# Optimization experiments

Measured on AMD Instinct MI355X. Metric: run time of the kernel, lower is better.

## Reference

```python
import jax, jax.numpy as jnp
import numpy as np

NS, NV = 48, 10            # scalar / vector multiplicities
IN_SIZE = NS + 3*NV + 3*NV + NS   # 156
N_EDGE_FEAT = 96
HIDDEN = 96
# weight shapes per output irrep: 0e:(58,48) 1o:(68,10) 1e:(68,10) 0o:(58,48)
W_SHAPES = [('0e', NS + NV, NS), ('1o', NS + 2*NV, NV), ('1e', 2*NV + NS, NV), ('0o', NV + NS, NS)]
WEIGHT_NUMEL = sum(a*b for _, a, b in W_SHAPES)  # 6928
N_NODES, N_EDGES = 10000, 50000


def setup_inputs() -> dict:
    key = jax.random.key(0)
    ks = jax.random.split(key, 9)
    node_attr = jax.random.normal(ks[0], (N_NODES, IN_SIZE), dtype=jnp.float32)
    edge_index = jax.random.randint(ks[1], (2, N_EDGES), 0, N_NODES)
    edge_attr = jax.random.normal(ks[2], (N_EDGES, N_EDGE_FEAT), dtype=jnp.float32)
    edge_sh = jax.random.normal(ks[3], (N_EDGES, 4), dtype=jnp.float32)
    s1 = 1.0 / np.sqrt(N_EDGE_FEAT)
    s2 = 1.0 / np.sqrt(HIDDEN)
    W1 = jax.random.normal(ks[4], (N_EDGE_FEAT, HIDDEN), dtype=jnp.float32) * s1
    b1 = jnp.zeros((HIDDEN,), dtype=jnp.float32)
    W2 = jax.random.normal(ks[5], (HIDDEN, WEIGHT_NUMEL), dtype=jnp.float32) * s2
    b2 = jnp.zeros((WEIGHT_NUMEL,), dtype=jnp.float32)
    return {'node_attr': node_attr, 'edge_index': edge_index, 'edge_attr': edge_attr,
            'edge_sh': edge_sh, 'W1': W1, 'b1': b1, 'W2': W2, 'b2': b2}


def _faster_tp(in_, sh, weight):
    # in_: [E, 156], sh: [E, 4], weight: [E, 6928]
    in_0e = in_[:, :NS]                                   # [E,48]
    in_1o = in_[:, NS:NS + 3*NV].reshape(-1, NV, 3)       # [E,10,3]
    in_1e = in_[:, NS + 3*NV:NS + 6*NV].reshape(-1, NV, 3)
    in_0o = in_[:, NS + 6*NV:]                            # [E,48]
    sh_0e = sh[:, 0]                                      # [E]
    sh_1o = sh[:, 1:]                                     # [E,3]
    inv_s3 = 1.0 / np.sqrt(3.0)
    inv_s2 = 1.0 / np.sqrt(2.0)

    out_0e = jnp.concatenate([
        in_0e * sh_0e[:, None],
        jnp.sum(in_1o * sh_1o[:, None, :], axis=-1) * inv_s3], axis=-1)      # [E,58]
    out_1o = jnp.concatenate([
        in_0e[:, :, None] * sh_1o[:, None, :],
        in_1o * sh_0e[:, None, None],
        jnp.cross(in_1e, sh_1o[:, None, :]) * inv_s2], axis=-2)              # [E,68,3]
    out_1e = jnp.concatenate([
        jnp.cross(in_1o, sh_1o[:, None, :]) * inv_s2,
        in_1e * sh_0e[:, None, None],
        in_0o[:, :, None] * sh_1o[:, None, :]], axis=-2)                     # [E,68,3]
    out_0o = jnp.concatenate([
        jnp.sum(in_1e * sh_1o[:, None, :], axis=-1) * inv_s3,
        in_0o * sh_0e[:, None]], axis=-1)                                    # [E,58]

    wd = {}
    start = 0
    for name, a, b in W_SHAPES:
        wd[name] = weight[:, start:start + a*b].reshape(-1, a, b) / np.sqrt(a)
        start += a*b

    o0e = jnp.einsum('ei,eio->eo', out_0e, wd['0e'])                 # [E,48]
    o1o = jnp.einsum('eic,eio->eoc', out_1o, wd['1o']).reshape(-1, 3*NV)
    o1e = jnp.einsum('eic,eio->eoc', out_1e, wd['1e']).reshape(-1, 3*NV)
    o0o = jnp.einsum('ei,eio->eo', out_0o, wd['0o'])                 # [E,48]
    return jnp.concatenate([o0e, o1o, o1e, o0o], axis=-1)           # [E,156]


def reference(node_attr, edge_index, edge_attr, edge_sh, W1, b1, W2, b2):
    edge_src, edge_dst = edge_index[0], edge_index[1]
    # edge MLP -> per-edge TP weights
    h = jax.nn.relu(edge_attr @ W1 + b1)
    w = h @ W2 + b2                                       # [E, 6928]
    tp = _faster_tp(node_attr[edge_dst], edge_sh, w)      # [E, 156]
    # scatter-mean over source nodes
    n = node_attr.shape[0]
    seg = jax.ops.segment_sum(tp, edge_src, num_segments=n)
    cnt = jax.ops.segment_sum(jnp.ones((tp.shape[0],), tp.dtype), edge_src, num_segments=n)
    out = seg / jnp.maximum(cnt, 1.0)[:, None]
    # residual (in/out sizes equal, so pad is a no-op)
    return out + node_attr
```

## Files before the change

### kernel.cpp

```cpp
#include <hip/hip_runtime.h>

#define NE 50000
#define NN 10000
#define KH 96
#define WN 6928
#define NTILE 484
#define IN_SZ 156
#define EPW 32

typedef __attribute__((ext_vector_type(8))) short short8;
typedef __attribute__((ext_vector_type(4))) float float4v;

__device__ __forceinline__ unsigned short f2bf(float x) {
  unsigned u = __float_as_uint(x);
  unsigned r = (u + 0x7FFFu + ((u >> 16) & 1u)) >> 16;
  return (unsigned short)r;
}
__device__ __forceinline__ float b2f(unsigned short u) {
  return __uint_as_float(((unsigned)u) << 16);
}

__device__ __forceinline__ void issue3(short8 (&B)[3], float &bv,
                                       const unsigned short* p, const float* pb) {
  asm volatile("global_load_dwordx4 %0, %4, off\n\t"
               "global_load_dwordx4 %1, %4, off offset:1024\n\t"
               "global_load_dwordx4 %2, %4, off offset:2048\n\t"
               "global_load_dword %3, %5, off"
               : "=&v"(B[0]), "=&v"(B[1]), "=&v"(B[2]), "=&v"(bv)
               : "v"(p), "v"(pb));
}
__device__ __forceinline__ void waitB8(short8 (&B)[3], float &bv) {
  asm volatile("s_waitcnt vmcnt(8)"
               : "+v"(B[0]), "+v"(B[1]), "+v"(B[2]), "+v"(bv));
}
__device__ __forceinline__ void waitB4(short8 (&B)[3], float &bv) {
  asm volatile("s_waitcnt vmcnt(4)"
               : "+v"(B[0]), "+v"(B[1]), "+v"(B[2]), "+v"(bv));
}
__device__ __forceinline__ void waitB0(short8 (&B)[3], float &bv) {
  asm volatile("s_waitcnt vmcnt(0)"
               : "+v"(B[0]), "+v"(B[1]), "+v"(B[2]), "+v"(bv));
}

__device__ __forceinline__ int col_of_np(int np) {
  if (np < 2784) return np;
  if (np < 3872) { int rel = np - 2784, i = rel >> 4, o = rel & 15; return (o < 10) ? 2784 + i * 10 + o : -1; }
  if (np < 4960) { int rel = np - 3872, i = rel >> 4, o = rel & 15; return (o < 10) ? 3464 + i * 10 + o : -1; }
  return 4144 + (np - 4960);
}

__global__ __launch_bounds__(256) void w1t_kernel(
    const float* __restrict__ W1, unsigned short* __restrict__ W1T)
{
  int j = blockIdx.x * 256 + threadIdx.x;
  if (j < KH * KH) {
    int c = j / KH, k = j - c * KH;
    W1T[c * KH + k] = f2bf(W1[k * KH + c]);
  }
}

__global__ __launch_bounds__(384) void mlp1_kernel(
    const float* __restrict__ edge_attr, const unsigned short* __restrict__ W1T,
    const float* __restrict__ b1, unsigned short* __restrict__ h_ext)
{
  const int tid = threadIdx.x;
  const int e0 = blockIdx.x * 16;
  const int w = tid >> 6, l = tid & 15, q = (tid >> 4) & 3;

  short8 a[3], b[3];
  #pragma unroll
  for (int s = 0; s < 3; ++s) {
    const float* pa = edge_attr + (size_t)(e0 + l) * KH + s * 32 + q * 8;
    float4 x = *(const float4*)pa, y = *(const float4*)(pa + 4);
    short8 t;
    t[0] = (short)f2bf(x.x); t[1] = (short)f2bf(x.y);
    t[2] = (short)f2bf(x.z); t[3] = (short)f2bf(x.w);
    t[4] = (short)f2bf(y.x); t[5] = (short)f2bf(y.y);
    t[6] = (short)f2bf(y.z); t[7] = (short)f2bf(y.w);
    a[s] = t;
    b[s] = *(const short8*)(W1T + (size_t)(w * 16 + l) * KH + s * 32 + q * 8);
  }
  float4v C = {0.f, 0.f, 0.f, 0.f};
  #pragma unroll
  for (int s = 0; s < 3; ++s)
    C = __builtin_amdgcn_mfma_f32_16x16x32_bf16(a[s], b[s], C, 0, 0, 0);

  float bv = b1[w * 16 + l];
  #pragma unroll
  for (int r = 0; r < 4; ++r)
    h_ext[(size_t)(e0 + q * 4 + r) * KH + w * 16 + l] = f2bf(fmaxf(C[r] + bv, 0.f));
}

__global__ __launch_bounds__(256) void w2pt_kernel(
    const float* __restrict__ W2, const float* __restrict__ b2,
    unsigned short* __restrict__ W2PT, float* __restrict__ b2PT)
{
  int gid = blockIdx.x * 256 + threadIdx.x;
  if (gid < NTILE * 192) {
    int lane = gid & 63, s = (gid >> 6) % 3, t = gid / 192;
    int l = lane & 15, q = lane >> 4;
    int c = col_of_np(t * 16 + l);
    int kbase = s * 32 + q * 8;
    unsigned short o8[8];
    #pragma unroll
    for (int j = 0; j < 8; ++j) {
      int k = kbase + j;
      float v = (c >= 0) ? W2[(size_t)k * WN + c] : 0.f;
      o8[j] = f2bf(v);
    }
    uint4 pk;
    pk.x = o8[0] | ((unsigned)o8[1] << 16);
    pk.y = o8[2] | ((unsigned)o8[3] << 16);
    pk.z = o8[4] | ((unsigned)o8[5] << 16);
    pk.w = o8[6] | ((unsigned)o8[7] << 16);
    *(uint4*)(W2PT + (size_t)gid * 8) = pk;
  } else {
    int j = gid - NTILE * 192;
    if (j < NTILE * 16) {
      int c = col_of_np(j);
      b2PT[j] = (c >= 0) ? b2[c] : 0.f;
    }
  }
}

__global__ __launch_bounds__(512, 4) void tp_kernel(
    const unsigned short* __restrict__ h_ext, const float* __restrict__ node_attr,
    const int* __restrict__ edge_index, const float* __restrict__ edge_sh,
    const unsigned short* __restrict__ W2PT, const float* __restrict__ b2PT,
    float* __restrict__ acc, int* __restrict__ icnt)
{
  __shared__ unsigned short sIn[EPW][160];
  __shared__ float sOut[EPW][IN_SZ];
  __shared__ unsigned short sF0[2][60][EPW];
  __shared__ unsigned short sF1[2][68][3][EPW];
  __shared__ float sShs[EPW][4];
  __shared__ int sSrc[EPW], sDst[EPW];

  const int tid = threadIdx.x;
  const int e0 = blockIdx.x * EPW;

  if (tid < EPW) {
    int ok = (e0 + tid) < NE;
    int s = ok ? edge_index[e0 + tid] : 0;
    int d = ok ? edge_index[NE + e0 + tid] : 0;
    sSrc[tid] = s; sDst[tid] = d;
    if (ok) atomicAdd(&icnt[s], 1);
  }
  if (tid >= 128 && tid < 256) {
    int t2 = tid - 128;
    int e = t2 >> 2, c = t2 & 3;
    sShs[e][c] = ((e0 + e) < NE) ? edge_sh[(size_t)(e0 + e) * 4 + c] : 0.f;
  }
  __syncthreads();

  for (int idx = tid; idx < EPW * IN_SZ; idx += 512) {
    int e = idx / IN_SZ, f = idx - e * IN_SZ;
    sIn[e][f] = f2bf(node_attr[(size_t)sDst[e] * IN_SZ + f]);
  }
  for (int idx = tid; idx < EPW * IN_SZ; idx += 512) (&sOut[0][0])[idx] = 0.f;
  __syncthreads();

  {
    const int e = tid >> 4, j = tid & 15;
    const float sh0 = sShs[e][0], sx = sShs[e][1], sy = sShs[e][2], sz = sShs[e][3];
    const float i3 = 0.57735026918962576f, i2 = 0.70710678118654752f;
    for (int i = j; i < 48; i += 16) {
      float v0 = b2f(sIn[e][i]), w0 = b2f(sIn[e][108 + i]);
      sF0[0][i][e] = f2bf(v0 * sh0);
      sF0[1][10 + i][e] = f2bf(w0 * sh0);
      sF1[0][i][0][e] = f2bf(v0 * sx); sF1[0][i][1][e] = f2bf(v0 * sy); sF1[0][i][2][e] = f2bf(v0 * sz);
      sF1[1][20 + i][0][e] = f2bf(w0 * sx); sF1[1][20 + i][1][e] = f2bf(w0 * sy); sF1[1][20 + i][2][e] = f2bf(w0 * sz);
    }
    if (j < 10) {
      const int v = j;
      float ax = b2f(sIn[e][48 + 3 * v]), ay = b2f(sIn[e][48 + 3 * v + 1]), az = b2f(sIn[e][48 + 3 * v + 2]);
      float bx = b2f(sIn[e][78 + 3 * v]), by = b2f(sIn[e][78 + 3 * v + 1]), bz = b2f(sIn[e][78 + 3 * v + 2]);
      sF0[0][48 + v][e] = f2bf((ax * sx + ay * sy + az * sz) * i3);
      sF0[1][v][e]      = f2bf((bx * sx + by * sy + bz * sz) * i3);
      sF1[0][48 + v][0][e] = f2bf(ax * sh0); sF1[0][48 + v][1][e] = f2bf(ay * sh0); sF1[0][48 + v][2][e] = f2bf(az * sh0);
      sF1[0][58 + v][0][e] = f2bf((by * sz - bz * sy) * i2);
      sF1[0][58 + v][1][e] = f2bf((bz * sx - bx * sz) * i2);
      sF1[0][58 + v][2][e] = f2bf((bx * sy - by * sx) * i2);
      sF1[1][v][0][e] = f2bf((ay * sz - az * sy) * i2);
      sF1[1][v][1][e] = f2bf((az * sx - ax * sz) * i2);
      sF1[1][v][2][e] = f2bf((ax * sy - ay * sx) * i2);
      sF1[1][10 + v][0][e] = f2bf(bx * sh0); sF1[1][10 + v][1][e] = f2bf(by * sh0); sF1[1][10 + v][2][e] = f2bf(bz * sh0);
    }
  }
  if (tid < 128) {
    int fam = tid >> 6, i = 58 + ((tid >> 5) & 1), e = tid & 31;
    sF0[fam][i][e] = 0;
  }
  __syncthreads();

  const int wv = tid >> 6, l = tid & 15, q = (tid >> 4) & 3;

  short8 Af[2][3];
  #pragma unroll
  for (int m = 0; m < 2; ++m) {
    const unsigned short* ar = h_ext + (size_t)(e0 + m * 16 + l) * KH + q * 8;
    #pragma unroll
    for (int s = 0; s < 3; ++s) Af[m][s] = *(const short8*)(ar + s * 32);
  }

  const unsigned short* wlane = W2PT + (size_t)(tid & 63) * 8;
  const float* blane = b2PT + l;

  if (wv < 4) {
    const int sf = wv >> 1;
    const int ibeg = (wv & 1) * 30;
    const int tb = sf ? 310 : 0;
    const int obase = sf ? 108 : 0;
    #pragma unroll 1
    for (int ob = 0; ob < 3; ++ob) {
      float a0[4] = {0.f, 0.f, 0.f, 0.f}, a1[4] = {0.f, 0.f, 0.f, 0.f};
      short8 Ba[3], Bb[3], Bc[3];
      float vA, vB, vC;
      auto taddr = [&](int ii) -> size_t {
        int i = ibeg + ii; if (i >= 58) i = ibeg;
        return (size_t)(tb + 3 * i + ob);
      };
      auto body = [&](const short8 (&B)[3], float bv, int ii) {
        int i = ibeg + ii;
        ushort4 f0 = *(const ushort4*)&sF0[sf][i][q * 4];
        ushort4 f1 = *(const ushort4*)&sF0[sf][i][16 + q * 4];
        float4v C0 = {bv, bv, bv, bv}, C1 = {bv, bv, bv, bv};
        #pragma unroll
        for (int s = 0; s < 3; ++s) {
          C0 = __builtin_amdgcn_mfma_f32_16x16x32_bf16(Af[0][s], B[s], C0, 0, 0, 0);
          C1 = __builtin_amdgcn_mfma_f32_16x16x32_bf16(Af[1][s], B[s], C1, 0, 0, 0);
        }
        a0[0] += C0[0] * b2f(f0.x); a0[1] += C0[1] * b2f(f0.y);
        a0[2] += C0[2] * b2f(f0.z); a0[3] += C0[3] * b2f(f0.w);
        a1[0] += C1[0] * b2f(f1.x); a1[1] += C1[1] * b2f(f1.y);
        a1[2] += C1[2] * b2f(f1.z); a1[3] += C1[3] * b2f(f1.w);
      };
      { size_t t = taddr(0); issue3(Ba, vA, wlane + t * 1536, blane + t * 16); }
      { size_t t = taddr(1); issue3(Bb, vB, wlane + t * 1536, blane + t * 16); }
      { size_t t = taddr(2); issue3(Bc, vC, wlane + t * 1536, blane + t * 16); }
      #pragma unroll 1
      for (int ii = 0; ii < 27; ii += 3) {
        waitB8(Ba, vA); body(Ba, vA, ii);
        { size_t t = taddr(ii + 3); issue3(Ba, vA, wlane + t * 1536, blane + t * 16); }
        waitB8(Bb, vB); body(Bb, vB, ii + 1);
        { size_t t = taddr(ii + 4); issue3(Bb, vB, wlane + t * 1536, blane + t * 16); }
        waitB8(Bc, vC); body(Bc, vC, ii + 2);
        { size_t t = taddr(ii + 5); issue3(Bc, vC, wlane + t * 1536, blane + t * 16); }
      }
      waitB8(Ba, vA); body(Ba, vA, 27);
      waitB4(Bb, vB); body(Bb, vB, 28);
      waitB0(Bc, vC); body(Bc, vC, 29);
      const int col = obase + ob * 16 + l;
      #pragma unroll
      for (int r = 0; r < 4; ++r) {
        unsafeAtomicAdd(&sOut[q * 4 + r][col], a0[r]);
        unsafeAtomicAdd(&sOut[16 + q * 4 + r][col], a1[r]);
      }
    }
  } else {
    const int vf = (wv >> 1) - 2;
    const int ibeg = (wv & 1) * 34;
    const int tb = vf ? 242 : 174;
    float r0[4][3] = {{0.f}}, r1[4][3] = {{0.f}};
    short8 Ba[3], Bb[3];
    float vA, vB;
    auto tadr = [&](int ii) -> size_t { return (size_t)(tb + ibeg + ii); };
    auto body = [&](const short8 (&B)[3], float bv, int ii) {
      int i = ibeg + ii;
      ushort4 g0[3], g1[3];
      #pragma unroll
      for (int cc = 0; cc < 3; ++cc) {
        g0[cc] = *(const ushort4*)&sF1[vf][i][cc][q * 4];
        g1[cc] = *(const ushort4*)&sF1[vf][i][cc][16 + q * 4];
      }
      float4v C0 = {bv, bv, bv, bv}, C1 = {bv, bv, bv, bv};
      #pragma unroll
      for (int s = 0; s < 3; ++s) {
        C0 = __builtin_amdgcn_mfma_f32_16x16x32_bf16(Af[0][s], B[s], C0, 0, 0, 0);
        C1 = __builtin_amdgcn_mfma_f32_16x16x32_bf16(Af[1][s], B[s], C1, 0, 0, 0);
      }
      #pragma unroll
      for (int cc = 0; cc < 3; ++cc) {
        r0[0][cc] += C0[0] * b2f(g0[cc].x); r0[1][cc] += C0[1] * b2f(g0[cc].y);
        r0[2][cc] += C0[2] * b2f(g0[cc].z); r0[3][cc] += C0[3] * b2f(g0[cc].w);
        r1[0][cc] += C1[0] * b2f(g1[cc].x); r1[1][cc] += C1[1] * b2f(g1[cc].y);
        r1[2][cc] += C1[2] * b2f(g1[cc].z); r1[3][cc] += C1[3] * b2f(g1[cc].w);
      }
    };
    { size_t t = tadr(0); issue3(Ba, vA, wlane + t * 1536, blane + t * 16); }
    { size_t t = tadr(1); issue3(Bb, vB, wlane + t * 1536, blane + t * 16); }
    #pragma unroll 1
    for (int ii = 0; ii < 32; ii += 2) {
      waitB4(Ba, vA); body(Ba, vA, ii);
      { size_t t = tadr(ii + 2); issue3(Ba, vA, wlane + t * 1536, blane + t * 16); }
      waitB4(Bb, vB); body(Bb, vB, ii + 1);
      { size_t t = tadr(ii + 3); issue3(Bb, vB, wlane + t * 1536, blane + t * 16); }
    }
    waitB4(Ba, vA); body(Ba, vA, 32);
    waitB0(Bb, vB); body(Bb, vB, 33);
    if (l < 10) {
      const int col = (vf ? 78 : 48) + 3 * l;
      #pragma unroll
      for (int r = 0; r < 4; ++r)
        #pragma unroll
        for (int cc = 0; cc < 3; ++cc) {
          unsafeAtomicAdd(&sOut[q * 4 + r][col + cc], r0[r][cc]);
          unsafeAtomicAdd(&sOut[16 + q * 4 + r][col + cc], r1[r][cc]);
        }
    }
  }
  __syncthreads();

  const float n58 = 0.13130643285972254f, n68 = 0.12126781251816650f;
  for (int idx = tid; idx < EPW * IN_SZ; idx += 512) {
    int e = idx / IN_SZ, o = idx - e * IN_SZ;
    if (e0 + e < NE) {
      float nrm = (o < 48 || o >= 108) ? n58 : n68;
      unsafeAtomicAdd(&acc[(size_t)sSrc[e] * IN_SZ + o], sOut[e][o] * nrm);
    }
  }
}

__global__ __launch_bounds__(256) void finalize_kernel(
    const float* __restrict__ acc, const int* __restrict__ icnt,
    const float* __restrict__ node_attr, float* __restrict__ out)
{
  int idx = blockIdx.x * 256 + threadIdx.x;
  if (idx < NN * IN_SZ) {
    int n = idx / IN_SZ;
    out[idx] = acc[idx] / fmaxf((float)icnt[n], 1.f) + node_attr[idx];
  }
}

extern "C" void kernel_launch(void* const* d_in, const int* in_sizes, int n_in,
                              void* d_out, int out_size, void* d_ws, size_t ws_size,
                              hipStream_t stream)
{
  const float* node_attr  = (const float*)d_in[0];
  const int*   edge_index = (const int*)d_in[1];
  const float* edge_attr  = (const float*)d_in[2];
  const float* edge_sh    = (const float*)d_in[3];
  const float* W1 = (const float*)d_in[4];
  const float* b1 = (const float*)d_in[5];
  const float* W2 = (const float*)d_in[6];
  const float* b2 = (const float*)d_in[7];
  float* out = (float*)d_out;

  unsigned short* h_ext = (unsigned short*)d_ws;
  unsigned short* W2PT  = h_ext + (size_t)50016 * KH;
  float* b2PT = (float*)(W2PT + (size_t)NTILE * 1536);
  float* acc  = b2PT + (size_t)NTILE * 16;
  int*   icnt = (int*)(acc + (size_t)NN * IN_SZ);
  unsigned short* W1T = (unsigned short*)(icnt + NN);

  w1t_kernel<<<(KH * KH + 255) / 256, 256, 0, stream>>>(W1, W1T);
  w2pt_kernel<<<(NTILE * 208 + 255) / 256, 256, 0, stream>>>(W2, b2, W2PT, b2PT);
  mlp1_kernel<<<NE / 16, 384, 0, stream>>>(edge_attr, W1T, b1, h_ext);
  hipMemsetAsync(acc, 0, (size_t)NN * IN_SZ * sizeof(float), stream);
  hipMemsetAsync(icnt, 0, (size_t)NN * sizeof(int), stream);
  hipMemsetAsync(h_ext + (size_t)NE * KH, 0, (size_t)16 * KH * sizeof(unsigned short), stream);
  tp_kernel<<<(NE + EPW - 1) / EPW, 512, 0, stream>>>(h_ext, node_attr, edge_index,
                                                      edge_sh, W2PT, b2PT, acc, icnt);
  finalize_kernel<<<(NN * IN_SZ + 255) / 256, 256, 0, stream>>>(acc, icnt, node_attr, out);
}
```

Before: 312.3 us.

## Quantize hidden activations and W2 to int8 and use i8 MFMA in TP kernel

Hidden activations are now quantized per edge and W2 per column to int8 with scales, and the per-edge weight GEMM uses int8 MFMA with int32 accumulation, followed by dequantization and bias. This halves weight and activation bytes and uses the higher-throughput int8 matrix path. The weight-transpose, W2 packing and memsets are also merged into a single prep kernel to cut launches. Occupancy hint changes from 4 to 2 waves per SIMD, and int8 quantization adds accuracy risk relative to bf16.

```diff
diff --git a/kernel.cpp b/kernel.cpp
--- a/kernel.cpp
+++ b/kernel.cpp
@@ -10,6 +10,9 @@
 
 typedef __attribute__((ext_vector_type(8))) short short8;
 typedef __attribute__((ext_vector_type(4))) float float4v;
+typedef __attribute__((ext_vector_type(4))) int int4v;
+typedef __attribute__((ext_vector_type(2))) float float2v;
+typedef __attribute__((ext_vector_type(2))) long long2v;
 
 __device__ __forceinline__ unsigned short f2bf(float x) {
   unsigned u = __float_as_uint(x);
@@ -19,27 +22,31 @@
 __device__ __forceinline__ float b2f(unsigned short u) {
   return __uint_as_float(((unsigned)u) << 16);
 }
-
-__device__ __forceinline__ void issue3(short8 (&B)[3], float &bv,
-                                       const unsigned short* p, const float* pb) {
-  asm volatile("global_load_dwordx4 %0, %4, off\n\t"
-               "global_load_dwordx4 %1, %4, off offset:1024\n\t"
-               "global_load_dwordx4 %2, %4, off offset:2048\n\t"
-               "global_load_dword %3, %5, off"
-               : "=&v"(B[0]), "=&v"(B[1]), "=&v"(B[2]), "=&v"(bv)
-               : "v"(p), "v"(pb));
-}
-__device__ __forceinline__ void waitB8(short8 (&B)[3], float &bv) {
-  asm volatile("s_waitcnt vmcnt(8)"
-               : "+v"(B[0]), "+v"(B[1]), "+v"(B[2]), "+v"(bv));
-}
-__device__ __forceinline__ void waitB4(short8 (&B)[3], float &bv) {
-  asm volatile("s_waitcnt vmcnt(4)"
-               : "+v"(B[0]), "+v"(B[1]), "+v"(B[2]), "+v"(bv));
-}
-__device__ __forceinline__ void waitB0(short8 (&B)[3], float &bv) {
-  asm volatile("s_waitcnt vmcnt(0)"
-               : "+v"(B[0]), "+v"(B[1]), "+v"(B[2]), "+v"(bv));
+__device__ __forceinline__ unsigned char q8(float x, float inv) {
+  return (unsigned char)(signed char)__float2int_rn(fminf(fmaxf(x * inv, -127.f), 127.f));
+}
+__device__ __forceinline__ unsigned p4(unsigned a, unsigned b, unsigned c, unsigned d) {
+  return a | (b << 8) | (c << 16) | (d << 24);
+}
+
+__device__ __forceinline__ void issueT(long2v &W01, long &W2f, float2v &bs,
+                                       const unsigned char* pA,
+                                       const unsigned char* pB,
+                                       const float* pbs) {
+  asm volatile("global_load_dwordx4 %0, %3, off\n\t"
+               "global_load_dwordx2 %1, %4, off\n\t"
+               "global_load_dwordx2 %2, %5, off"
+               : "=&v"(W01), "=&v"(W2f), "=&v"(bs)
+               : "v"(pA), "v"(pB), "v"(pbs));
+}
+__device__ __forceinline__ void waitT6(long2v &W01, long &W2f, float2v &bs) {
+  asm volatile("s_waitcnt vmcnt(6)" : "+v"(W01), "+v"(W2f), "+v"(bs));
+}
+__device__ __forceinline__ void waitT3(long2v &W01, long &W2f, float2v &bs) {
+  asm volatile("s_waitcnt vmcnt(3)" : "+v"(W01), "+v"(W2f), "+v"(bs));
+}
+__device__ __forceinline__ void waitT0(long2v &W01, long &W2f, float2v &bs) {
+  asm volatile("s_waitcnt vmcnt(0)" : "+v"(W01), "+v"(W2f), "+v"(bs));
 }
 
 __device__ __forceinline__ int col_of_np(int np) {
@@ -49,23 +56,83 @@
   return 4144 + (np - 4960);
 }
 
-__global__ __launch_bounds__(256) void w1t_kernel(
-    const float* __restrict__ W1, unsigned short* __restrict__ W1T)
+#define R0 (NTILE * 16)
+#define R1 (R0 + KH * KH)
+#define R2 (R1 + NN * IN_SZ / 4)
+#define R3 (R2 + NN / 4)
+#define R4 (R3 + 96)
+#define R5 (R4 + 4)
+__global__ __launch_bounds__(256) void prep_kernel(
+    const float* __restrict__ W2, const float* __restrict__ b2,
+    const float* __restrict__ W1,
+    unsigned char* __restrict__ W2PT8, float2v* __restrict__ bscPT,
+    unsigned short* __restrict__ W1T,
+    float* __restrict__ acc, int* __restrict__ icnt,
+    unsigned char* __restrict__ h8, float* __restrict__ hscale)
 {
-  int j = blockIdx.x * 256 + threadIdx.x;
-  if (j < KH * KH) {
+  int gid = blockIdx.x * 256 + threadIdx.x;
+  if (gid < R0) {
+    int np = gid, t = np >> 4, l = np & 15;
+    int c = col_of_np(np);
+    float m = 0.f;
+    if (c >= 0) {
+      #pragma unroll 1
+      for (int k = 0; k < KH; ++k) m = fmaxf(m, fabsf(W2[(size_t)k * WN + c]));
+    }
+    float sc = m / 127.f;
+    float inv = (m > 0.f) ? 127.f / m : 0.f;
+    float2v bs; bs.x = (c >= 0) ? b2[c] : 0.f; bs.y = sc;
+    bscPT[np] = bs;
+    #pragma unroll 1
+    for (int qq = 0; qq < 4; ++qq) {
+      unsigned char bb[24];
+      #pragma unroll
+      for (int j = 0; j < 8; ++j) {
+        int k0 = qq * 8 + j;
+        bb[j]      = q8((c >= 0) ? W2[(size_t)k0 * WN + c] : 0.f, inv);
+        bb[8 + j]  = q8((c >= 0) ? W2[(size_t)(32 + k0) * WN + c] : 0.f, inv);
+        bb[16 + j] = q8((c >= 0) ? W2[(size_t)(64 + k0) * WN + c] : 0.f, inv);
+      }
+      uint4 pa;
+      pa.x = p4(bb[0], bb[1], bb[2], bb[3]);
+      pa.y = p4(bb[4], bb[5], bb[6], bb[7]);
+      pa.z = p4(bb[8], bb[9], bb[10], bb[11]);
+      pa.w = p4(bb[12], bb[13], bb[14], bb[15]);
+      *(uint4*)(W2PT8 + (size_t)t * 1536 + (qq * 16 + l) * 16) = pa;
+      uint2 pb;
+      pb.x = p4(bb[16], bb[17], bb[18], bb[19]);
+      pb.y = p4(bb[20], bb[21], bb[22], bb[23]);
+      *(uint2*)(W2PT8 + (size_t)t * 1536 + 1024 + (qq * 16 + l) * 8) = pb;
+    }
+  } else if (gid < R1) {
+    int j = gid - R0;
     int c = j / KH, k = j - c * KH;
     W1T[c * KH + k] = f2bf(W1[k * KH + c]);
+  } else if (gid < R2) {
+    uint4 z = {0, 0, 0, 0};
+    ((uint4*)acc)[gid - R1] = z;
+  } else if (gid < R3) {
+    uint4 z = {0, 0, 0, 0};
+    ((uint4*)icnt)[gid - R2] = z;
+  } else if (gid < R4) {
+    uint4 z = {0, 0, 0, 0};
+    ((uint4*)(h8 + (size_t)NE * KH))[gid - R3] = z;
+  } else if (gid < R5) {
+    uint4 z = {0, 0, 0, 0};
+    ((uint4*)(hscale + NE))[gid - R4] = z;
   }
 }
 
 __global__ __launch_bounds__(384) void mlp1_kernel(
     const float* __restrict__ edge_attr, const unsigned short* __restrict__ W1T,
-    const float* __restrict__ b1, unsigned short* __restrict__ h_ext)
+    const float* __restrict__ b1, unsigned char* __restrict__ h8,
+    float* __restrict__ hscale)
 {
+  __shared__ unsigned rmax[16];
   const int tid = threadIdx.x;
   const int e0 = blockIdx.x * 16;
   const int w = tid >> 6, l = tid & 15, q = (tid >> 4) & 3;
+  if (tid < 16) rmax[tid] = 0;
 
   short8 a[3], b[3];
   #pragma unroll
@@ -86,47 +153,32 @@
     C = __builtin_amdgcn_mfma_f32_16x16x32_bf16(a[s], b[s], C, 0, 0, 0);
 
   float bv = b1[w * 16 + l];
-  #pragma unroll
-  for (int r = 0; r < 4; ++r)
-    h_ext[(size_t)(e0 + q * 4 + r) * KH + w * 16 + l] = f2bf(fmaxf(C[r] + bv, 0.f));
-}
-
-__global__ __launch_bounds__(256) void w2pt_kernel(
-    const float* __restrict__ W2, const float* __restrict__ b2,
-    unsigned short* __restrict__ W2PT, float* __restrict__ b2PT)
-{
-  int gid = blockIdx.x * 256 + threadIdx.x;
-  if (gid < NTILE * 192) {
-    int lane = gid & 63, s = (gid >> 6) % 3, t = gid / 192;
-    int l = lane & 15, q = lane >> 4;
-    int c = col_of_np(t * 16 + l);
-    int kbase = s * 32 + q * 8;
-    unsigned short o8[8];
+  float v[4];
+  #pragma unroll
+  for (int r = 0; r < 4; ++r) v[r] = fmaxf(C[r] + bv, 0.f);
+  __syncthreads();
+  #pragma unroll
+  for (int r = 0; r < 4; ++r) atomicMax(&rmax[q * 4 + r], __float_as_uint(v[r]));
+  __syncthreads();
+  #pragma unroll
+  for (int r = 0; r < 4; ++r) {
+    float m = __uint_as_float(rmax[q * 4 + r]);
+    float inv = (m > 0.f) ? 127.f / m : 0.f;
+    h8[(size_t)(e0 + q * 4 + r) * KH + w * 16 + l] =
+        (unsigned char)__float2int_rn(v[r] * inv);
+  }
+  if (w == 0 && l == 0) {
     #pragma unroll
-    for (int j = 0; j < 8; ++j) {
-      int k = kbase + j;
-      float v = (c >= 0) ? W2[(size_t)k * WN + c] : 0.f;
-      o8[j] = f2bf(v);
-    }
-    uint4 pk;
-    pk.x = o8[0] | ((unsigned)o8[1] << 16);
-    pk.y = o8[2] | ((unsigned)o8[3] << 16);
-    pk.z = o8[4] | ((unsigned)o8[5] << 16);
-    pk.w = o8[6] | ((unsigned)o8[7] << 16);
-    *(uint4*)(W2PT + (size_t)gid * 8) = pk;
-  } else {
-    int j = gid - NTILE * 192;
-    if (j < NTILE * 16) {
-      int c = col_of_np(j);
-      b2PT[j] = (c >= 0) ? b2[c] : 0.f;
-    }
-  }
-}
-
-__global__ __launch_bounds__(512, 4) void tp_kernel(
-    const unsigned short* __restrict__ h_ext, const float* __restrict__ node_attr,
+    for (int r = 0; r < 4; ++r)
+      hscale[e0 + q * 4 + r] = __uint_as_float(rmax[q * 4 + r]) / 127.f;
+  }
+}
+
+__global__ __launch_bounds__(512, 2) void tp_kernel(
+    const unsigned char* __restrict__ h8, const float* __restrict__ node_attr,
     const int* __restrict__ edge_index, const float* __restrict__ edge_sh,
-    const unsigned short* __restrict__ W2PT, const float* __restrict__ b2PT,
+    const unsigned char* __restrict__ W2PT8, const float2v* __restrict__ bscPT,
+    const float* __restrict__ hscale,
     float* __restrict__ acc, int* __restrict__ icnt)
 {
   __shared__ unsigned short sIn[EPW][160];
@@ -195,16 +247,47 @@
 
   const int wv = tid >> 6, l = tid & 15, q = (tid >> 4) & 3;
 
-  short8 Af[2][3];
+  long Af[2][3];
+  float se0[4], se1[4];
   #pragma unroll
   for (int m = 0; m < 2; ++m) {
-    const unsigned short* ar = h_ext + (size_t)(e0 + m * 16 + l) * KH + q * 8;
+    const unsigned char* ar = h8 + (size_t)(e0 + m * 16 + l) * KH + q * 8;
     #pragma unroll
-    for (int s = 0; s < 3; ++s) Af[m][s] = *(const short8*)(ar + s * 32);
-  }
-
-  const unsigned short* wlane = W2PT + (size_t)(tid & 63) * 8;
-  const float* blane = b2PT + l;
+    for (int s = 0; s < 3; ++s) Af[m][s] = *(const long*)(ar + s * 32);
+  }
+  #pragma unroll
+  for (int r = 0; r < 4; ++r) {
+    se0[r] = hscale[e0 + q * 4 + r];
+    se1[r] = hscale[e0 + 16 + q * 4 + r];
+  }
+
+  const unsigned char* wlaneA = W2PT8 + (size_t)(tid & 63) * 16;
+  const unsigned char* wlaneB = W2PT8 + 1024 + (size_t)(tid & 63) * 8;
+  const float* bslane = (const float*)(bscPT + l);
+
+  auto sbody = [&](float (&a0)[4], float (&a1)[4],
+                   const long2v &W01, const long &W2f, const float2v &bs,
+                   int sf, int i) {
+    ushort4 f0 = *(const ushort4*)&sF0[sf][i][q * 4];
+    ushort4 f1 = *(const ushort4*)&sF0[sf][i][16 + q * 4];
+    int4v C0 = {0, 0, 0, 0}, C1 = {0, 0, 0, 0};
+    C0 = __builtin_amdgcn_mfma_i32_16x16x32_i8(Af[0][0], W01.x, C0, 0, 0, 0);
+    C1 = __builtin_amdgcn_mfma_i32_16x16x32_i8(Af[1][0], W01.x, C1, 0, 0, 0);
+    C0 = __builtin_amdgcn_mfma_i32_16x16x32_i8(Af[0][1], W01.y, C0, 0, 0, 0);
+    C1 = __builtin_amdgcn_mfma_i32_16x16x32_i8(Af[1][1], W01.y, C1, 0, 0, 0);
+    C0 = __builtin_amdgcn_mfma_i32_16x16x32_i8(Af[0][2], W2f, C0, 0, 0, 0);
+    C1 = __builtin_amdgcn_mfma_i32_16x16x32_i8(Af[1][2], W2f, C1, 0, 0, 0);
+    const float bv = bs.x, sc = bs.y;
+    float u;
+    u = fmaf((float)C0[0], sc * se0[0], bv); a0[0] = fmaf(u, b2f(f0.x), a0[0]);
+    u = fmaf((float)C0[1], sc * se0[1], bv); a0[1] = fmaf(u, b2f(f0.y), a0[1]);
+    u = fmaf((float)C0[2], sc * se0[2], bv); a0[2] = fmaf(u, b2f(f0.z), a0[2]);
+    u = fmaf((float)C0[3], sc * se0[3], bv); a0[3] = fmaf(u, b2f(f0.w), a0[3]);
+    u = fmaf((float)C1[0], sc * se1[0], bv); a1[0] = fmaf(u, b2f(f1.x), a1[0]);
+    u = fmaf((float)C1[1], sc * se1[1], bv); a1[1] = fmaf(u, b2f(f1.y), a1[1]);
+    u = fmaf((float)C1[2], sc * se1[2], bv); a1[2] = fmaf(u, b2f(f1.z), a1[2]);
+    u = fmaf((float)C1[3], sc * se1[3], bv); a1[3] = fmaf(u, b2f(f1.w), a1[3]);
+  };
 
   if (wv < 4) {
     const int sf = wv >> 1;
@@ -214,46 +297,30 @@
     #pragma unroll 1
     for (int ob = 0; ob < 3; ++ob) {
       float a0[4] = {0.f, 0.f, 0.f, 0.f}, a1[4] = {0.f, 0.f, 0.f, 0.f};
-      short8 Ba[3], Bb[3], Bc[3];
-      float vA, vB, vC;
-      auto taddr = [&](int ii) -> size_t {
+      long2v Wa01, Wb01, Wc01; long Wa2, Wb2, Wc2; float2v vA, vB, vC;
+      auto tadr = [&](int ii) -> size_t {
         int i = ibeg + ii; if (i >= 58) i = ibeg;
         return (size_t)(tb + 3 * i + ob);
       };
-      auto body = [&](const short8 (&B)[3], float bv, int ii) {
-        int i = ibeg + ii;
-        ushort4 f0 = *(const ushort4*)&sF0[sf][i][q * 4];
-        ushort4 f1 = *(const ushort4*)&sF0[sf][i][16 + q * 4];
-        float4v C0 = {bv, bv, bv, bv}, C1 = {bv, bv, bv, bv};
-        #pragma unroll
-        for (int s = 0; s < 3; ++s) {
-          C0 = __builtin_amdgcn_mfma_f32_16x16x32_bf16(Af[0][s], B[s], C0, 0, 0, 0);
-          C1 = __builtin_amdgcn_mfma_f32_16x16x32_bf16(Af[1][s], B[s], C1, 0, 0, 0);
-        }
-        a0[0] += C0[0] * b2f(f0.x); a0[1] += C0[1] * b2f(f0.y);
-        a0[2] += C0[2] * b2f(f0.z); a0[3] += C0[3] * b2f(f0.w);
-        a1[0] += C1[0] * b2f(f1.x); a1[1] += C1[1] * b2f(f1.y);
-        a1[2] += C1[2] * b2f(f1.z); a1[3] += C1[3] * b2f(f1.w);
-      };
-      { size_t t = taddr(0); issue3(Ba, vA, wlane + t * 1536, blane + t * 16); }
-      { size_t t = taddr(1); issue3(Bb, vB, wlane + t * 1536, blane + t * 16); }
-      { size_t t = taddr(2); issue3(Bc, vC, wlane + t * 1536, blane + t * 16); }
+      { size_t t = tadr(0); issueT(Wa01, Wa2, vA, wlaneA + t * 1536, wlaneB + t * 1536, bslane + t * 32); }
+      { size_t t = tadr(1); issueT(Wb01, Wb2, vB, wlaneA + t * 1536, wlaneB + t * 1536, bslane + t * 32); }
+      { size_t t = tadr(2); issueT(Wc01, Wc2, vC, wlaneA + t * 1536, wlaneB + t * 1536, bslane + t * 32); }
       #pragma unroll 1
       for (int ii = 0; ii < 27; ii += 3) {
-        waitB8(Ba, vA); body(Ba, vA, ii);
-        { size_t t = taddr(ii + 3); issue3(Ba, vA, wlane + t * 1536, blane + t * 16); }
-        waitB8(Bb, vB); body(Bb, vB, ii + 1);
-        { size_t t = taddr(ii + 4); issue3(Bb, vB, wlane + t * 1536, blane + t * 16); }
-        waitB8(Bc, vC); body(Bc, vC, ii + 2);
-        { size_t t = taddr(ii + 5); issue3(Bc, vC, wlane + t * 1536, blane + t * 16); }
-      }
-      waitB8(Ba, vA); body(Ba, vA, 27);
-      waitB4(Bb, vB); body(Bb, vB, 28);
-      waitB0(Bc, vC); body(Bc, vC, 29);
+        waitT6(Wa01, Wa2, vA); sbody(a0, a1, Wa01, Wa2, vA, sf, ibeg + ii);
+        { size_t t = tadr(ii + 3); issueT(Wa01, Wa2, vA, wlaneA + t * 1536, wlaneB + t * 1536, bslane + t * 32); }
+        waitT6(Wb01, Wb2, vB); sbody(a0, a1, Wb01, Wb2, vB, sf, ibeg + ii + 1);
+        { size_t t = tadr(ii + 4); issueT(Wb01, Wb2, vB, wlaneA + t * 1536, wlaneB + t * 1536, bslane + t * 32); }
+        waitT6(Wc01, Wc2, vC); sbody(a0, a1, Wc01, Wc2, vC, sf, ibeg + ii + 2);
+        { size_t t = tadr(ii + 5); issueT(Wc01, Wc2, vC, wlaneA + t * 1536, wlaneB + t * 1536, bslane + t * 32); }
+      }
+      waitT6(Wa01, Wa2, vA); sbody(a0, a1, Wa01, Wa2, vA, sf, ibeg + 27);
+      waitT3(Wb01, Wb2, vB); sbody(a0, a1, Wb01, Wb2, vB, sf, ibeg + 28);
+      waitT0(Wc01, Wc2, vC); sbody(a0, a1, Wc01, Wc2, vC, sf, ibeg + 29);
       const int col = obase + ob * 16 + l;
       #pragma unroll
       for (int r = 0; r < 4; ++r) {
-        unsafeAtomicAdd(&sOut[q * 4 + r][col], a0[r]);
+        unsafeAtomicAdd(&sOut[q * 4 + r][col],      a0[r]);
         unsafeAtomicAdd(&sOut[16 + q * 4 + r][col], a1[r]);
       }
     }
@@ -262,10 +329,9 @@
     const int ibeg = (wv & 1) * 34;
     const int tb = vf ? 242 : 174;
     float r0[4][3] = {{0.f}}, r1[4][3] = {{0.f}};
-    short8 Ba[3], Bb[3];
-    float vA, vB;
+    long2v Wa01, Wb01; long Wa2, Wb2; float2v vA, vB;
     auto tadr = [&](int ii) -> size_t { return (size_t)(tb + ibeg + ii); };
-    auto body = [&](const short8 (&B)[3], float bv, int ii) {
+    auto vbody = [&](const long2v &W01, const long &W2f, const float2v &bs, int ii) {
       int i = ibeg + ii;
       ushort4 g0[3], g1[3];
       #pragma unroll
@@ -273,31 +339,43 @@
         g0[cc] = *(const ushort4*)&sF1[vf][i][cc][q * 4];
         g1[cc] = *(const ushort4*)&sF1[vf][i][cc][16 + q * 4];
       }
-      float4v C0 = {bv, bv, bv, bv}, C1 = {bv, bv, bv, bv};
-      #pragma unroll
-      for (int s = 0; s < 3; ++s) {
-        C0 = __builtin_amdgcn_mfma_f32_16x16x32_bf16(Af[0][s], B[s], C0, 0, 0, 0);
-        C1 = __builtin_amdgcn_mfma_f32_16x16x32_bf16(Af[1][s], B[s], C1, 0, 0, 0);
+      int4v C0 = {0, 0, 0, 0}, C1 = {0, 0, 0, 0};
+      C0 = __builtin_amdgcn_mfma_i32_16x16x32_i8(Af[0][0], W01.x, C0, 0, 0, 0);
+      C1 = __builtin_amdgcn_mfma_i32_16x16x32_i8(Af[1][0], W01.x, C1, 0, 0, 0);
+      C0 = __builtin_amdgcn_mfma_i32_16x16x32_i8(Af[0][1], W01.y, C0, 0, 0, 0);
+      C1 = __builtin_amdgcn_mfma_i32_16x16x32_i8(Af[1][1], W01.y, C1, 0, 0, 0);
+      C0 = __builtin_amdgcn_mfma_i32_16x16x32_i8(Af[0][2], W2f, C0, 0, 0, 0);
+      C1 = __builtin_amdgcn_mfma_i32_16x16x32_i8(Af[1][2], W2f, C1, 0, 0, 0);
+      const float bv = bs.x, sc = bs.y;
+      float u0[4], u1[4];
+      #pragma unroll
+      for (int r = 0; r < 4; ++r) {
+        u0[r] = fmaf((float)C0[r], sc * se0[r], bv);
+        u1[r] = fmaf((float)C1[r], sc * se1[r], bv);
       }
       #pragma unroll
       for (int cc = 0; cc < 3; ++cc) {
-        r0[0][cc] += C0[0] * b2f(g0[cc].x); r0[1][cc] += C0[1] * b2f(g0[cc].y);
-        r0[2][cc] += C0[2] * b2f(g0[cc].z); r0[3][cc] += C0[3] * b2f(g0[cc].w);
-        r1[0][cc] += C1[0] * b2f(g1[cc].x); r1[1][cc] += C1[1] * b2f(g1[cc].y);
-        r1[2][cc] += C1[2] * b2f(g1[cc].z); r1[3][cc] += C1[3] * b2f(g1[cc].w);
+        r0[0][cc] = fmaf(u0[0], b2f(g0[cc].x), r0[0][cc]);
+        r0[1][cc] = fmaf(u0[1], b2f(g0[cc].y), r0[1][cc]);
+        r0[2][cc] = fmaf(u0[2], b2f(g0[cc].z), r0[2][cc]);
+        r0[3][cc] = fmaf(u0[3], b2f(g0[cc].w), r0[3][cc]);
+        r1[0][cc] = fmaf(u1[0], b2f(g1[cc].x), r1[0][cc]);
+        r1[1][cc] = fmaf(u1[1], b2f(g1[cc].y), r1[1][cc]);
+        r1[2][cc] = fmaf(u1[2], b2f(g1[cc].z), r1[2][cc]);
+        r1[3][cc] = fmaf(u1[3], b2f(g1[cc].w), r1[3][cc]);
       }
     };
-    { size_t t = tadr(0); issue3(Ba, vA, wlane + t * 1536, blane + t * 16); }
-    { size_t t = tadr(1); issue3(Bb, vB, wlane + t * 1536, blane + t * 16); }
+    { size_t t = tadr(0); issueT(Wa01, Wa2, vA, wlaneA + t * 1536, wlaneB + t * 1536, bslane + t * 32); }
+    { size_t t = tadr(1); issueT(Wb01, Wb2, vB, wlaneA + t * 1536, wlaneB + t * 1536, bslane + t * 32); }
     #pragma unroll 1
     for (int ii = 0; ii < 32; ii += 2) {
-      waitB4(Ba, vA); body(Ba, vA, ii);
-      { size_t t = tadr(ii + 2); issue3(Ba, vA, wlane + t * 1536, blane + t * 16); }
-      waitB4(Bb, vB); body(Bb, vB, ii + 1);
-      { size_t t = tadr(ii + 3); issue3(Bb, vB, wlane + t * 1536, blane + t * 16); }
-    }
-    waitB4(Ba, vA); body(Ba, vA, 32);
-    waitB0(Bb, vB); body(Bb, vB, 33);
+      waitT3(Wa01, Wa2, vA); vbody(Wa01, Wa2, vA, ii);
+      { size_t t = tadr(ii + 2); issueT(Wa01, Wa2, vA, wlaneA + t * 1536, wlaneB + t * 1536, bslane + t * 32); }
+      waitT3(Wb01, Wb2, vB); vbody(Wb01, Wb2, vB, ii + 1);
+      { size_t t = tadr(ii + 3); issueT(Wb01, Wb2, vB, wlaneA + t * 1536, wlaneB + t * 1536, bslane + t * 32); }
+    }
+    waitT3(Wa01, Wa2, vA); vbody(Wa01, Wa2, vA, 32);
+    waitT0(Wb01, Wb2, vB); vbody(Wb01, Wb2, vB, 33);
     if (l < 10) {
       const int col = (vf ? 78 : 48) + 3 * l;
       #pragma unroll
@@ -346,20 +424,19 @@
   const float* b2 = (const float*)d_in[7];
   float* out = (float*)d_out;
 
-  unsigned short* h_ext = (unsigned short*)d_ws;
-  unsigned short* W2PT  = h_ext + (size_t)50016 * KH;
-  float* b2PT = (float*)(W2PT + (size_t)NTILE * 1536);
-  float* acc  = b2PT + (size_t)NTILE * 16;
+  unsigned char* h8    = (unsigned char*)d_ws;
+  unsigned char* W2PT8 = h8 + (size_t)50016 * KH;
+  float2v* bscPT = (float2v*)(W2PT8 + (size_t)NTILE * 1536);
+  float* hscale = (float*)(bscPT + NTILE * 16);
+  float* acc  = hscale + 50016;
   int*   icnt = (int*)(acc + (size_t)NN * IN_SZ);
   unsigned short* W1T = (unsigned short*)(icnt + NN);
 
-  w1t_kernel<<<(KH * KH + 255) / 256, 256, 0, stream>>>(W1, W1T);
-  w2pt_kernel<<<(NTILE * 208 + 255) / 256, 256, 0, stream>>>(W2, b2, W2PT, b2PT);
-  mlp1_kernel<<<NE / 16, 384, 0, stream>>>(edge_attr, W1T, b1, h_ext);
-  hipMemsetAsync(acc, 0, (size_t)NN * IN_SZ * sizeof(float), stream);
-  hipMemsetAsync(icnt, 0, (size_t)NN * sizeof(int), stream);
-  hipMemsetAsync(h_ext + (size_t)NE * KH, 0, (size_t)16 * KH * sizeof(unsigned short), stream);
-  tp_kernel<<<(NE + EPW - 1) / EPW, 512, 0, stream>>>(h_ext, node_attr, edge_index,
-                                                      edge_sh, W2PT, b2PT, acc, icnt);
+  prep_kernel<<<(R5 + 255) / 256, 256, 0, stream>>>(W2, b2, W1, W2PT8, bscPT, W1T,
+                                                    acc, icnt, h8, hscale);
+  mlp1_kernel<<<NE / 16, 384, 0, stream>>>(edge_attr, W1T, b1, h8, hscale);
+  tp_kernel<<<(NE + EPW - 1) / EPW, 512, 0, stream>>>(h8, node_attr, edge_index,
+                                                      edge_sh, W2PT8, bscPT, hscale,
+                                                      acc, icnt);
   finalize_kernel<<<(NN * IN_SZ + 255) / 256, 256, 0, stream>>>(acc, icnt, node_attr, out);
 }
```

Result: slower. 389.2 us (+24.6%).
